# Performance work log

Hardware: AMD Instinct MI355X
Metric: run time of the kernel (lower is better)

The kernel has to match this reference:

```python
import jax, jax.numpy as jnp
import numpy as np
from jax import lax

B, S, T = 64, 64, 32
VE = VD = 32000
E = H = 256
L = 2


def _cell(x, h, c, Wih, Whh, b):
    # PyTorch LSTM gate order: i, f, g, o
    g = x @ Wih.T + h @ Whh.T + b  # [B, 4H]
    i, f, gg, o = jnp.split(g, 4, axis=-1)
    c2 = jax.nn.sigmoid(f) * c + jax.nn.sigmoid(i) * jnp.tanh(gg)
    h2 = jax.nn.sigmoid(o) * jnp.tanh(c2)
    return h2, c2


def _stack_step(x, h, c, Wih, Whh, b):
    # x: [B, E]; h, c: [L, B, H]. Stacked LSTM, dropout is identity at inference.
    hs, cs = [], []
    inp = x
    for l in range(h.shape[0]):
        h2, c2 = _cell(inp, h[l], c[l], Wih[l], Whh[l], b[l])
        hs.append(h2); cs.append(c2)
        inp = h2
    return jnp.stack(hs), jnp.stack(cs), inp


def _encode(tokens, emb, Wih, Whh, b):
    x = emb[tokens]  # [B, S, E]
    bsz = tokens.shape[0]
    h0 = jnp.zeros((L, bsz, H), x.dtype)
    c0 = jnp.zeros((L, bsz, H), x.dtype)

    def step(carry, xt):
        h, c = carry
        h, c, _ = _stack_step(xt, h, c, Wih, Whh, b)
        return (h, c), None

    (h, c), _ = lax.scan(step, (h0, c0), x.transpose(1, 0, 2))
    return h, c


def setup_inputs():
    key = jax.random.key(0)
    ks = jax.random.split(key, 12)
    sd = lambda k, shape: (jax.random.normal(k, shape, dtype=jnp.float32) * 0.05)
    return {
        "input_seq": jax.random.randint(ks[0], (B, S), 0, VE),
        "target_seq": jax.random.randint(ks[1], (B, T), 0, VD),
        "enc_emb": sd(ks[2], (VE, E)),
        "dec_emb": sd(ks[3], (VD, E)),
        "enc_Wih": sd(ks[4], (L, 4 * H, E)),
        "enc_Whh": sd(ks[5], (L, 4 * H, H)),
        "enc_b": sd(ks[6], (L, 4 * H)),
        "dec_Wih": sd(ks[7], (L, 4 * H, E)),
        "dec_Whh": sd(ks[8], (L, 4 * H, H)),
        "dec_b": sd(ks[9], (L, 4 * H)),
        "W_out": sd(ks[10], (VD, H)),
        "b_out": sd(ks[11], (VD,)),
    }


def reference(input_seq, target_seq, enc_emb, dec_emb, enc_Wih, enc_Whh, enc_b,
              dec_Wih, dec_Whh, dec_b, W_out, b_out):
    h, c = _encode(input_seq, enc_emb, enc_Wih, enc_Whh, enc_b)
    bsz, tlen = target_seq.shape
    # dec_in buffer; position 0 is BOS token target_seq[:, 0]; rest filled greedily
    buf0 = jnp.zeros((bsz, tlen), dtype=target_seq.dtype).at[:, 0].set(target_seq[:, 0])
    pos = jnp.arange(tlen)

    def outer(carry, t):
        h, c, buf = carry
        x = dec_emb[buf]  # [B, T, E] -- whole growing prefix re-fed, as in source

        def inner(carry, inp):
            hh, cc = carry
            xt, p = inp
            h2, c2, _ = _stack_step(xt, hh, cc, dec_Wih, dec_Whh, dec_b)
            m = p <= t  # only positions up to current prefix length update state
            hh = jnp.where(m, h2, hh)
            cc = jnp.where(m, c2, cc)
            return (hh, cc), None

        (h, c), _ = lax.scan(inner, (h, c), (x.transpose(1, 0, 2), pos))
        out_top = h[-1]  # LSTM output at last real position t
        pred = out_top @ W_out.T + b_out  # [B, V]
        nxt = jnp.argmax(pred, axis=-1).astype(buf.dtype)
        buf = buf.at[:, t + 1].set(nxt)
        return (h, c, buf), pred

    (_, _, _), preds = lax.scan(outer, (h, c, buf0), jnp.arange(tlen - 1))
    return preds.transpose(1, 0, 2)  # [B, T-1, V]
```

## Files before the change

### kernel.cpp

```cpp
#include <hip/hip_runtime.h>
#include <math.h>


#define B     64
#define SLEN  64
#define TLEN  32
#define HID   256
#define EMBD  256
#define G4    1024
#define VOC   32000
#define NPRED 31
#define FBASE 64
#define FS    16

typedef unsigned long long u64;

__device__ __forceinline__ float sigf(float x){ return 1.0f/(1.0f+__expf(-x)); }

__device__ __forceinline__ void gstoref(float* p, float v){
  __hip_atomic_store(p, v, __ATOMIC_RELAXED, __HIP_MEMORY_SCOPE_AGENT);
}
__device__ __forceinline__ void gstorei(int* p, int v){
  __hip_atomic_store(p, v, __ATOMIC_RELAXED, __HIP_MEMORY_SCOPE_AGENT);
}
__device__ __forceinline__ float gloadf(const float* p){
  return __hip_atomic_load(p, __ATOMIC_RELAXED, __HIP_MEMORY_SCOPE_AGENT);
}
__device__ __forceinline__ int gload32(const int* p){
  return __hip_atomic_load(p, __ATOMIC_RELAXED, __HIP_MEMORY_SCOPE_AGENT);
}

__global__ void k_zero(int* __restrict__ p){
  p[blockIdx.x*1024 + threadIdx.x] = 0;
}

__global__ __launch_bounds__(256) void k_tr(const float* __restrict__ src,
                                            float* __restrict__ dst){
  __shared__ float t[64][65];
  const int r0 = blockIdx.x*64, c0 = blockIdx.y*64;
  const int lr = threadIdx.x>>6, lc = threadIdx.x&63;
  #pragma unroll
  for (int i=0;i<16;i++){
    int r = lr + i*4;
    t[r][lc] = src[(size_t)(r0+r)*256 + c0+lc];
  }
  __syncthreads();
  #pragma unroll
  for (int i=0;i<16;i++){
    int c = lr + i*4;
    dst[(size_t)(c0+c)*1024 + r0+lc] = t[lc][c];
  }
}

__global__ __launch_bounds__(256) void k_xproj(
    const int* __restrict__ tok, int tok_stride, int pos0,
    const float* __restrict__ emb, const float* __restrict__ W,
    const float* __restrict__ b0, float* __restrict__ out)
{
  __shared__ float xT[128][64];
  const int tid  = threadIdx.x;
  const int lane = tid & 63;
  const int wv   = __builtin_amdgcn_readfirstlane(tid >> 6);
  const int pos  = pos0 + blockIdx.y;
  const int jbase= blockIdx.x*32 + wv*8;

  const int rS = tid >> 2, klane = tid & 3;
  const int tokrow = tok[rS*tok_stride + pos];
  const float* xsrc = emb + (size_t)tokrow*EMBD;

  float acc[8];
  #pragma unroll
  for (int jj=0;jj<8;jj++) acc[jj]=0.f;

  for (int c=0;c<2;c++){
    __syncthreads();
    #pragma unroll
    for (int i=0;i<32;i++){
      int k = klane + 4*i;
      xT[k][rS] = xsrc[c*128 + k];
    }
    __syncthreads();
    for (int kc=0;kc<8;kc++){
      float x[16];
      #pragma unroll
      for (int i=0;i<16;i++) x[i] = xT[kc*16+i][lane];
      #pragma unroll
      for (int jj=0;jj<8;jj++){
        const float* Wp = W + (size_t)(jbase+jj)*EMBD + c*128 + kc*16;
        float s = 0.f;
        #pragma unroll
        for (int i=0;i<16;i++) s += Wp[i]*x[i];
        acc[jj] += s;
      }
    }
  }
  #pragma unroll
  for (int jj=0;jj<8;jj++){
    int j = jbase+jj;
    out[((size_t)pos*64 + lane)*G4 + j] = acc[jj] + b0[j];
  }
}

__device__ __forceinline__ float4 dotpart(const float4* __restrict__ Wq,
                                          const float* __restrict__ hs,
                                          int kq, int jg){
  float ax=0.f, ay=0.f, az=0.f, aw=0.f;
  const float4* __restrict__ hq = (const float4*)(hs + (kq<<6));
  const float4* __restrict__ w  = Wq + (size_t)(kq<<6)*256 + jg;
  #pragma unroll 4
  for (int kk=0; kk<16; ++kk){
    float4 h4 = hq[kk];
    float4 w0 = w[0];
    float4 w1 = w[256];
    float4 w2 = w[512];
    float4 w3 = w[768];
    ax += w0.x*h4.x; ay += w0.y*h4.x; az += w0.z*h4.x; aw += w0.w*h4.x;
    ax += w1.x*h4.y; ay += w1.y*h4.y; az += w1.z*h4.y; aw += w1.w*h4.y;
    ax += w2.x*h4.z; ay += w2.y*h4.z; az += w2.z*h4.z; aw += w2.w*h4.z;
    ax += w3.x*h4.w; ay += w3.y*h4.w; az += w3.z*h4.w; aw += w3.w*h4.w;
    w += 1024;
  }
  return make_float4(ax,ay,az,aw);
}

__global__ __launch_bounds__(1024) void k_pipe(
    const float* __restrict__ xp, int nsteps,
    const float* __restrict__ WT0, const float* __restrict__ WT1i,
    const float* __restrict__ WT1h, const float* __restrict__ b1,
    float* __restrict__ h0P, float* __restrict__ h1P,
    float* __restrict__ c0P, float* __restrict__ c1P,
    float* __restrict__ h0R, float* __restrict__ p1R,
    int* __restrict__ fA, int* __restrict__ fB1, int* __restrict__ fB2,
    int fbase, int initzero)
{
  __shared__ __align__(16) float part[4][4096];
  __shared__ float xps[1024];
  __shared__ __align__(16) float hloc[256];
  __shared__ float padL[4096];
  const int tid  = threadIdx.x;
  const int kq   = tid >> 8, jg = tid & 255;
  const int role = blockIdx.x >> 6;
  const int r    = blockIdx.x & 63;
  if (nsteps < 0){ padL[tid] = xp[tid]; h0R[tid] = padL[tid ^ 1]; }

  if (role == 0){
    float c0 = 0.f;
    if (tid < HID){
      if (initzero){ c0 = 0.f; hloc[tid] = 0.f; }
      else { c0 = c0P[tid*64 + r]; hloc[tid] = h0P[tid*64 + r]; }
    }
    __syncthreads();
    const float4* W4 = (const float4*)WT0;
    for (int q = 0; q < nsteps; ++q){
      float xv = xp[((size_t)q*64 + r)*G4 + tid];
      if (tid == 0 && q >= 4){
        int tgt = fbase + q - 3, g = 0;
        while (gload32(fB1 + r*FS) < tgt && ++g < (1<<24)) {}
      }
      float4 a = dotpart(W4, hloc, kq, jg);
      xps[tid] = xv;
      *(float4*)&part[kq][jg<<2] = a;
      __syncthreads();
      if (tid < HID){
        float g0 = part[0][tid]+part[1][tid]+part[2][tid]+part[3][tid] + xps[tid];
        float g1 = part[0][HID+tid]+part[1][HID+tid]+part[2][HID+tid]+part[3][HID+tid] + xps[HID+tid];
        float g2 = part[0][2*HID+tid]+part[1][2*HID+tid]+part[2][2*HID+tid]+part[3][2*HID+tid] + xps[2*HID+tid];
        float g3 = part[0][3*HID+tid]+part[1][3*HID+tid]+part[2][3*HID+tid]+part[3][3*HID+tid] + xps[3*HID+tid];
        c0 = sigf(g1)*c0 + sigf(g0)*tanhf(g2);
        float h = sigf(g3)*tanhf(c0);
        hloc[tid] = h;
        gstoref(h0R + (q&3)*16384 + r*256 + tid, h);
        asm volatile("s_waitcnt vmcnt(0)" ::: "memory");
      }
      __syncthreads();
      if (tid == 0) gstorei(fA + r*FS, fbase + q + 1);
    }
    if (tid < HID){ c0P[tid*64 + r] = c0; h0P[tid*64 + r] = hloc[tid]; }
  }
  else if (role == 1){
    const float4* W4 = (const float4*)WT1i;
    for (int q = 0; q < nsteps; ++q){
      if (tid == 0){
        int tgt = fbase + q + 1, g = 0;
        while (gload32(fA + r*FS) < tgt && ++g < (1<<24)) {}
        if (q >= 4){
          int t2 = fbase + q - 3; g = 0;
          while (gload32(fB2 + r*FS) < t2 && ++g < (1<<24)) {}
        }
      }
      __syncthreads();
      if (tid < HID) hloc[tid] = gloadf(h0R + (q&3)*16384 + r*256 + tid);
      __syncthreads();
      float4 a = dotpart(W4, hloc, kq, jg);
      *(float4*)&part[kq][jg<<2] = a;
      __syncthreads();
      float p = part[0][tid]+part[1][tid]+part[2][tid]+part[3][tid];
      gstoref(p1R + (q&3)*65536 + r*1024 + tid, p);
      asm volatile("s_waitcnt vmcnt(0)" ::: "memory");
      __syncthreads();
      if (tid == 0) gstorei(fB1 + r*FS, fbase + q + 1);
    }
  }
  else {
    float c1 = 0.f, bb0=0.f, bb1=0.f, bb2=0.f, bb3=0.f;
    if (tid < HID){
      bb0 = b1[tid]; bb1 = b1[HID+tid]; bb2 = b1[2*HID+tid]; bb3 = b1[3*HID+tid];
      if (initzero){ c1 = 0.f; hloc[tid] = 0.f; }
      else { c1 = c1P[tid*64 + r]; hloc[tid] = h1P[tid*64 + r]; }
    }
    __syncthreads();
    const float4* W4 = (const float4*)WT1h;
    for (int q = 0; q < nsteps; ++q){
      if (tid == 0){
        int tgt = fbase + q + 1, g = 0;
        while (gload32(fB1 + r*FS) < tgt && ++g < (1<<24)) {}
      }
      __syncthreads();
      xps[tid] = gloadf(p1R + (q&3)*65536 + r*1024 + tid);
      asm volatile("s_waitcnt vmcnt(0)" ::: "memory");
      __syncthreads();
      if (tid == 0) gstorei(fB2 + r*FS, fbase + q + 1);
      float4 a = dotpart(W4, hloc, kq, jg);
      *(float4*)&part[kq][jg<<2] = a;
      __syncthreads();
      if (tid < HID){
        float g0 = part[0][tid]+part[1][tid]+part[2][tid]+part[3][tid] + xps[tid] + bb0;
        float g1 = part[0][HID+tid]+part[1][HID+tid]+part[2][HID+tid]+part[3][HID+tid] + xps[HID+tid] + bb1;
        float g2 = part[0][2*HID+tid]+part[1][2*HID+tid]+part[2][2*HID+tid]+part[3][2*HID+tid] + xps[2*HID+tid] + bb2;
        float g3 = part[0][3*HID+tid]+part[1][3*HID+tid]+part[2][3*HID+tid]+part[3][3*HID+tid] + xps[3*HID+tid] + bb3;
        c1 = sigf(g1)*c1 + sigf(g0)*tanhf(g2);
        float h = sigf(g3)*tanhf(c1);
        hloc[tid] = h;
        if (q == nsteps-1) h1P[tid*64 + r] = h;
      }
      __syncthreads();
    }
    if (tid < HID) c1P[tid*64 + r] = c1;
  }
}

__global__ __launch_bounds__(1024) void k_megadec(
    float* xp,
    const float* __restrict__ WT0, const float* __restrict__ WT1i,
    const float* __restrict__ WT1h, const float* __restrict__ b1,
    const float* __restrict__ Wih0, const float* __restrict__ b0,
    const float* __restrict__ emb,
    const float* __restrict__ Wout, const float* __restrict__ bout,
    float* __restrict__ dout,
    const float* __restrict__ h0P, const float* __restrict__ h1P,
    const float* __restrict__ c0P, const float* __restrict__ c1P,
    float* __restrict__ h0R, float* __restrict__ p1R, float* __restrict__ h1R,
    float* __restrict__ pPv, int* __restrict__ pPi,
    int* __restrict__ flags)
{
  __shared__ __align__(16) float part[4][4096];
  __shared__ float xps[1024];
  __shared__ __align__(16) float hloc[256];
  __shared__ int   iscr[1024];
  __shared__ float htp[256*65];

  int* fA = flags;          int* fB1 = flags + 1024;  int* fB2 = flags + 2048;
  int* fH = flags + 3072;   int* fP  = flags + 4096;  int* fX  = flags + 5120;

  const int tid  = threadIdx.x;
  const int lane = tid & 63;
  const int wv   = __builtin_amdgcn_readfirstlane(tid >> 6);
  const int kq   = tid >> 8, jg = tid & 255;
  const int xcd  = blockIdx.x & 7;
  const int role = xcd >> 1;
  const int r    = ((xcd & 1) << 5) | (blockIdx.x >> 3);

  if (role == 0){
    float c0 = 0.f;
    if (tid < HID){ c0 = c0P[tid*64 + r]; hloc[tid] = h0P[tid*64 + r]; }
    __syncthreads();
    const float4* W4 = (const float4*)WT0;
    int cum = 0;
    for (int t = 0; t < NPRED; ++t)
    for (int p = 0; p <= t; ++p, ++cum){
      if (wv == 0){
        if (lane == 0 && cum >= 4){
          int tgt = FBASE + cum - 3, g = 0;
          while (gload32(fB1 + r*FS) < tgt && ++g < (1<<24)) {}
        }
        if (p == t && t >= 1){
          int g = 0;
          while (!__all(gload32(fX + lane*FS) >= t) && ++g < (1<<24)) {}
        }
      }
      __syncthreads();
      const float* xa = xp + ((size_t)p*64 + r)*G4 + tid;
      float xv = (p == t) ? gloadf(xa) : *xa;
      float4 a = dotpart(W4, hloc, kq, jg);
      xps[tid] = xv;
      *(float4*)&part[kq][jg<<2] = a;
      __syncthreads();
      if (tid < HID){
        float g0 = part[0][tid]+part[1][tid]+part[2][tid]+part[3][tid] + xps[tid];
        float g1 = part[0][HID+tid]+part[1][HID+tid]+part[2][HID+tid]+part[3][HID+tid] + xps[HID+tid];
        float g2 = part[0][2*HID+tid]+part[1][2*HID+tid]+part[2][2*HID+tid]+part[3][2*HID+tid] + xps[2*HID+tid];
        float g3 = part[0][3*HID+tid]+part[1][3*HID+tid]+part[2][3*HID+tid]+part[3][3*HID+tid] + xps[3*HID+tid];
        c0 = sigf(g1)*c0 + sigf(g0)*tanhf(g2);
        float h = sigf(g3)*tanhf(c0);
        hloc[tid] = h;
        gstoref(h0R + (cum&3)*16384 + r*256 + tid, h);
        asm volatile("s_waitcnt vmcnt(0)" ::: "memory");
      }
      __syncthreads();
      if (tid == 0) gstorei(fA + r*FS, FBASE + cum + 1);
    }
  }
  else if (role == 1){
    const float4* W4 = (const float4*)WT1i;
    int cum = 0;
    for (int t = 0; t < NPRED; ++t)
    for (int p = 0; p <= t; ++p, ++cum){
      if (tid == 0){
        int tgt = FBASE + cum + 1, g = 0;
        while (gload32(fA + r*FS) < tgt && ++g < (1<<24)) {}
        if (cum >= 4){
          int t2 = FBASE + cum - 3; g = 0;
          while (gload32(fB2 + r*FS) < t2 && ++g < (1<<24)) {}
        }
      }
      __syncthreads();
      if (tid < HID) hloc[tid] = gloadf(h0R + (cum&3)*16384 + r*256 + tid);
      __syncthreads();
      float4 a = dotpart(W4, hloc, kq, jg);
      *(float4*)&part[kq][jg<<2] = a;
      __syncthreads();
      float pp = part[0][tid]+part[1][tid]+part[2][tid]+part[3][tid];
      gstoref(p1R + (cum&3)*65536 + r*1024 + tid, pp);
      asm volatile("s_waitcnt vmcnt(0)" ::: "memory");
      __syncthreads();
      if (tid == 0) gstorei(fB1 + r*FS, FBASE + cum + 1);
    }
  }
  else if (role == 2){
    float c1 = 0.f, bb0=0.f, bb1=0.f, bb2=0.f, bb3=0.f;
    if (tid < HID){
      bb0 = b1[tid]; bb1 = b1[HID+tid]; bb2 = b1[2*HID+tid]; bb3 = b1[3*HID+tid];
      c1 = c1P[tid*64 + r]; hloc[tid] = h1P[tid*64 + r];
    }
    __syncthreads();
    const float4* W4 = (const float4*)WT1h;
    int cum = 0;
    for (int t = 0; t < NPRED; ++t)
    for (int p = 0; p <= t; ++p, ++cum){
      if (tid == 0){
        int tgt = FBASE + cum + 1, g = 0;
        while (gload32(fB1 + r*FS) < tgt && ++g < (1<<24)) {}
      }
      __syncthreads();
      xps[tid] = gloadf(p1R + (cum&3)*65536 + r*1024 + tid);
      asm volatile("s_waitcnt vmcnt(0)" ::: "memory");
      __syncthreads();
      if (tid == 0) gstorei(fB2 + r*FS, FBASE + cum + 1);
      float4 a = dotpart(W4, hloc, kq, jg);
      *(float4*)&part[kq][jg<<2] = a;
      __syncthreads();
      if (tid < HID){
        float g0 = part[0][tid]+part[1][tid]+part[2][tid]+part[3][tid] + xps[tid] + bb0;
        float g1 = part[0][HID+tid]+part[1][HID+tid]+part[2][HID+tid]+part[3][HID+tid] + xps[HID+tid] + bb1;
        float g2 = part[0][2*HID+tid]+part[1][2*HID+tid]+part[2][2*HID+tid]+part[3][2*HID+tid] + xps[2*HID+tid] + bb2;
        float g3 = part[0][3*HID+tid]+part[1][3*HID+tid]+part[2][3*HID+tid]+part[3][3*HID+tid] + xps[3*HID+tid] + bb3;
        c1 = sigf(g1)*c1 + sigf(g0)*tanhf(g2);
        float h = sigf(g3)*tanhf(c1);
        hloc[tid] = h;
      }
      __syncthreads();
      if (p == t){
        if (tid == 0 && t >= 2){
          int g = 0;
          while (gload32(fP) < t - 1 && ++g < (1<<24)) {}
        }
        if (wv == 1 && t >= 2){
          int g = 0;
          while (!__all(gload32(fP + lane*FS) >= t-1) && ++g < (1<<24)) {}
        }
        __syncthreads();
        if (tid < HID){
          gstoref(h1R + (t&1)*16384 + r*256 + tid, hloc[tid]);
          asm volatile("s_waitcnt vmcnt(0)" ::: "memory");
        }
        __syncthreads();
        if (tid == 0) gstorei(fH + r*FS, t + 1);
      }
    }
  }
  else {
    const int v  = r;
    const int v0 = v * 500;
    const int rr = tid >> 4;
    const int jl = tid & 15;
    const float b0v = b0[v*16 + jl];

    for (int t = 0; t < NPRED; ++t){
      if (wv == 0){
        int g = 0;
        while (!__all(gload32(fH + lane*FS) >= t+1) && ++g < (1<<24))
          __builtin_amdgcn_s_sleep(8);
      }
      __syncthreads();
      {
        const float* src = h1R + (size_t)(t&1)*16384;
        #pragma unroll
        for (int i=0;i<16;i++){
          int idx = tid + i*1024;
          float vl = gloadf(src + idx);
          htp[(idx & 255)*65 + (idx >> 8)] = vl;
        }
      }
      __syncthreads();
      float best = -INFINITY; int bi = 0x7fffffff;
      for (int ib = 0; ib < 4; ++ib){
        float acc[8];
        #pragma unroll
        for (int jj=0;jj<8;jj++){
          int i = ib*8+jj;
          acc[jj] = (wv + 16*i < 500) ? bout[v0 + wv + 16*i] : 0.f;
        }
        for (int kc = 0; kc < 16; ++kc){
          float x[16];
          #pragma unroll
          for (int u=0;u<16;u++) x[u] = htp[(kc*16+u)*65 + lane];
          #pragma unroll
          for (int jj=0;jj<8;jj++){
            int i = ib*8+jj;
            if (wv + 16*i < 500){
              const float* Wp = Wout + (size_t)(v0 + wv + 16*i)*HID + kc*16;
              #pragma unroll
              for (int u=0;u<16;u++) acc[jj] += Wp[u]*x[u];
            }
          }
        }
        #pragma unroll
        for (int jj=0;jj<8;jj++){
          int i = ib*8+jj;
          if (wv + 16*i < 500){
            int vv = v0 + wv + 16*i;
            dout[((size_t)lane*NPRED + t)*VOC + vv] = acc[jj];
            if (acc[jj] > best){ best = acc[jj]; bi = vv; }
          }
        }
      }
      xps[wv*64 + lane] = best; iscr[wv*64 + lane] = bi;
      __syncthreads();
      if (wv == 0){
        float bb = xps[lane]; int bbi = iscr[lane];
        #pragma unroll
        for (int w=1; w<16; w++){
          float vl = xps[w*64+lane]; int ii = iscr[w*64+lane];
          if (vl > bb || (vl == bb && ii < bbi)){ bb = vl; bbi = ii; }
        }
        gstoref(pPv + (t&1)*4096 + v*64 + lane, bb);
        gstorei(pPi + (t&1)*4096 + v*64 + lane, bbi);
        asm volatile("s_waitcnt vmcnt(0)" ::: "memory");
      }
      __syncthreads();
      if (tid == 0) gstorei(fP + v*FS, t + 1);
      if (t == NPRED-1) continue;

      if (wv == 0){
        int g = 0;
        while (!__all(gload32(fP + lane*FS) >= t+1) && ++g < (1<<24)) {}
        float bb = -INFINITY; int bbi = 0x7fffffff;
        for (int vs = 0; vs < 64; ++vs){
          float vl = gloadf(pPv + (t&1)*4096 + vs*64 + lane);
          int  ii  = gload32(pPi + (t&1)*4096 + vs*64 + lane);
          if (vl > bb || (vl == bb && ii < bbi)){ bb = vl; bbi = ii; }
        }
        iscr[lane] = bbi;
      }
      __syncthreads();
      {
        #pragma unroll
        for (int i=0;i<16;i++){
          int idx = tid + i*1024;
          int k2 = idx >> 6, r2 = idx & 63;
          int tk = iscr[r2];
          htp[k2*65 + r2] = emb[(size_t)tk*EMBD + k2];
        }
      }
      __syncthreads();
      {
        int j = v*16 + jl;
        const float* Wj = Wih0 + (size_t)j*EMBD;
        float acc = b0v;
        #pragma unroll 16
        for (int k2=0;k2<256;k2++) acc += Wj[k2]*htp[k2*65 + rr];
        gstoref(xp + ((size_t)(t+1)*64 + rr)*G4 + v*16 + jl, acc);
        asm volatile("s_waitcnt vmcnt(0)" ::: "memory");
      }
      __syncthreads();
      if (tid == 0) gstorei(fX + v*FS, t + 1);
    }
  }
}

extern "C" void kernel_launch(void* const* d_in, const int* in_sizes, int n_in,
                              void* d_out, int out_size, void* d_ws, size_t ws_size,
                              hipStream_t stream)
{
  const int*   input_seq  = (const int*)d_in[0];
  const int*   target_seq = (const int*)d_in[1];
  const float* enc_emb = (const float*)d_in[2];
  const float* dec_emb = (const float*)d_in[3];
  const float* enc_Wih = (const float*)d_in[4];
  const float* enc_Whh = (const float*)d_in[5];
  const float* enc_b   = (const float*)d_in[6];
  const float* dec_Wih = (const float*)d_in[7];
  const float* dec_Whh = (const float*)d_in[8];
  const float* dec_b   = (const float*)d_in[9];
  const float* W_out   = (const float*)d_in[10];
  const float* b_out   = (const float*)d_in[11];
  float* out = (float*)d_out;

  float* ws   = (float*)d_ws;
  float* xp_e = ws;
  float* xp_d = xp_e + (size_t)SLEN*64*G4;
  float* h0P  = xp_d + (size_t)TLEN*64*G4;
  float* h1P  = h0P + HID*64;
  float* c0P  = h1P + HID*64;
  float* c1P  = c0P + HID*64;
  float* h0R  = c1P + HID*64;
  float* p1R  = h0R + 4*16384;
  float* h1R  = p1R + 4*65536;
  float* pPv  = h1R + 2*16384;
  int*   pPi  = (int*)(pPv + 2*4096);
  int*   flags= (int*)(pPi + 2*4096);
  float* WT0  = (float*)(flags + 6144);
  float* WT1i = WT0  + HID*G4;
  float* WT1h = WT1i + HID*G4;

  k_zero<<<6, 1024, 0, stream>>>(flags);

  dim3 trg(16, 4);
  k_tr<<<trg, 256, 0, stream>>>(enc_Whh,                   WT0);
  k_tr<<<trg, 256, 0, stream>>>(enc_Wih + (size_t)G4*EMBD, WT1i);
  k_tr<<<trg, 256, 0, stream>>>(enc_Whh + (size_t)G4*HID,  WT1h);
  k_xproj<<<dim3(32, SLEN), 256, 0, stream>>>(input_seq, SLEN, 0, enc_emb,
        enc_Wih, enc_b, xp_e);
  k_pipe<<<192, 1024, 0, stream>>>(xp_e, SLEN,
        WT0, WT1i, WT1h, enc_b + G4,
        h0P, h1P, c0P, c1P, h0R, p1R,
        flags, flags + 1024, flags + 2048, 0, 1);

  k_tr<<<trg, 256, 0, stream>>>(dec_Whh,                   WT0);
  k_tr<<<trg, 256, 0, stream>>>(dec_Wih + (size_t)G4*EMBD, WT1i);
  k_tr<<<trg, 256, 0, stream>>>(dec_Whh + (size_t)G4*HID,  WT1h);
  k_xproj<<<dim3(32, 1), 256, 0, stream>>>(target_seq, TLEN, 0, dec_emb,
        dec_Wih, dec_b, xp_d);

  k_megadec<<<256, 1024, 0, stream>>>(xp_d,
        WT0, WT1i, WT1h, dec_b + G4,
        dec_Wih, dec_b, dec_emb, W_out, b_out, out,
        h0P, h1P, c0P, c1P,
        h0R, p1R, h1R, pPv, pPi, flags);
}
```

Measured before the change: 9.060 ms.

## Funnel cross-block flag polling through a single aggregator block

Many-to-many flag polling between the recurrence blocks and the 64 vocabulary/projection blocks is replaced by aggregation in block v==0. That block alone polls all fH, fP and fX flags, then publishes single go flags (fGo, fTok, fXGo) plus the argmax token vector. The other blocks spin on one word instead of 64 strided flags, cutting global polling traffic and contention. The cost is an extra serial hop through block 0 on each handoff, which adds latency on the critical path.

Result: slower. 9.494 ms (+4.8%).

```diff
diff --git a/kernel.cpp b/kernel.cpp
--- a/kernel.cpp
+++ b/kernel.cpp
@@ -259,8 +259,10 @@
   __shared__ int   iscr[1024];
   __shared__ float htp[256*65];
 
-  int* fA = flags;          int* fB1 = flags + 1024;  int* fB2 = flags + 2048;
-  int* fH = flags + 3072;   int* fP  = flags + 4096;  int* fX  = flags + 5120;
+  int* fA  = flags;          int* fB1 = flags + 1024;  int* fB2 = flags + 2048;
+  int* fH  = flags + 3072;   int* fP  = flags + 4096;  int* fX  = flags + 5120;
+  int* fGo = flags + 6144;   int* fTok= flags + 6160;  int* fXGo= flags + 6176;
+  int* tokG= flags + 6656;
 
   const int tid  = threadIdx.x;
   const int lane = tid & 63;
@@ -278,17 +280,18 @@
     int cum = 0;
     for (int t = 0; t < NPRED; ++t)
     for (int p = 0; p <= t; ++p, ++cum){
-      if (wv == 0){
-        if (lane == 0 && cum >= 4){
+      if (tid == 0){
+        if (cum >= 4){
           int tgt = FBASE + cum - 3, g = 0;
           while (gload32(fB1 + r*FS) < tgt && ++g < (1<<24)) {}
         }
         if (p == t && t >= 1){
           int g = 0;
-          while (!__all(gload32(fX + lane*FS) >= t) && ++g < (1<<24)) {}
-        }
-      }
-      __syncthreads();
+          while (gload32(fXGo) < t && ++g < (1<<24)) {}
+        }
+      }
+      __syncthreads();
+      asm volatile("" ::: "memory");
       const float* xa = xp + ((size_t)p*64 + r)*G4 + tid;
       float xv = (p == t) ? gloadf(xa) : *xa;
       float4 a = dotpart(W4, hloc, kq, jg);
@@ -372,13 +375,10 @@
       if (p == t){
         if (tid == 0 && t >= 2){
           int g = 0;
-          while (gload32(fP) < t - 1 && ++g < (1<<24)) {}
-        }
-        if (wv == 1 && t >= 2){
-          int g = 0;
-          while (!__all(gload32(fP + lane*FS) >= t-1) && ++g < (1<<24)) {}
-        }
-        __syncthreads();
+          while (gload32(fTok) < t - 1 && ++g < (1<<24)) {}
+        }
+        __syncthreads();
+        asm volatile("" ::: "memory");
         if (tid < HID){
           gstoref(h1R + (t&1)*16384 + r*256 + tid, hloc[tid]);
           asm volatile("s_waitcnt vmcnt(0)" ::: "memory");
@@ -396,12 +396,23 @@
     const float b0v = b0[v*16 + jl];
 
     for (int t = 0; t < NPRED; ++t){
-      if (wv == 0){
-        int g = 0;
-        while (!__all(gload32(fH + lane*FS) >= t+1) && ++g < (1<<24))
-          __builtin_amdgcn_s_sleep(8);
-      }
-      __syncthreads();
+      if (v == 0){
+        if (wv == 0){
+          int g = 0;
+          while (!__all(gload32(fH + lane*FS) >= t+1) && ++g < (1<<24))
+            __builtin_amdgcn_s_sleep(4);
+        }
+        __syncthreads();
+        if (tid == 0) gstorei(fGo, t + 1);
+      } else {
+        if (tid == 0){
+          int g = 0;
+          while (gload32(fGo) < t + 1 && ++g < (1<<24))
+            __builtin_amdgcn_s_sleep(8);
+        }
+        __syncthreads();
+      }
+      asm volatile("" ::: "memory");
       {
         const float* src = h1R + (size_t)(t&1)*16384;
         #pragma unroll
@@ -461,18 +472,33 @@
       if (tid == 0) gstorei(fP + v*FS, t + 1);
       if (t == NPRED-1) continue;
 
-      if (wv == 0){
-        int g = 0;
-        while (!__all(gload32(fP + lane*FS) >= t+1) && ++g < (1<<24)) {}
-        float bb = -INFINITY; int bbi = 0x7fffffff;
-        for (int vs = 0; vs < 64; ++vs){
-          float vl = gloadf(pPv + (t&1)*4096 + vs*64 + lane);
-          int  ii  = gload32(pPi + (t&1)*4096 + vs*64 + lane);
-          if (vl > bb || (vl == bb && ii < bbi)){ bb = vl; bbi = ii; }
-        }
-        iscr[lane] = bbi;
-      }
-      __syncthreads();
+      if (v == 0){
+        if (wv == 0){
+          int g = 0;
+          while (!__all(gload32(fP + lane*FS) >= t+1) && ++g < (1<<24)) {}
+          float bb = -INFINITY; int bbi = 0x7fffffff;
+          for (int vs = 0; vs < 64; ++vs){
+            float vl = gloadf(pPv + (t&1)*4096 + vs*64 + lane);
+            int  ii  = gload32(pPi + (t&1)*4096 + vs*64 + lane);
+            if (vl > bb || (vl == bb && ii < bbi)){ bb = vl; bbi = ii; }
+          }
+          iscr[lane] = bbi;
+          gstorei(tokG + lane, bbi);
+          asm volatile("s_waitcnt vmcnt(0)" ::: "memory");
+        }
+        __syncthreads();
+        if (tid == 0) gstorei(fTok, t + 1);
+      } else {
+        if (tid == 0){
+          int g = 0;
+          while (gload32(fTok) < t + 1 && ++g < (1<<24))
+            __builtin_amdgcn_s_sleep(2);
+        }
+        __syncthreads();
+        asm volatile("" ::: "memory");
+        if (tid < 64) iscr[tid] = gload32(tokG + tid);
+        __syncthreads();
+      }
       {
         #pragma unroll
         for (int i=0;i<16;i++){
@@ -494,6 +520,14 @@
       }
       __syncthreads();
       if (tid == 0) gstorei(fX + v*FS, t + 1);
+      if (v == 0){
+        if (wv == 0){
+          int g = 0;
+          while (!__all(gload32(fX + lane*FS) >= t+1) && ++g < (1<<24)) {}
+        }
+        __syncthreads();
+        if (tid == 0) gstorei(fXGo, t + 1);
+      }
     }
   }
 }
@@ -529,11 +563,11 @@
   float* pPv  = h1R + 2*16384;
   int*   pPi  = (int*)(pPv + 2*4096);
   int*   flags= (int*)(pPi + 2*4096);
-  float* WT0  = (float*)(flags + 6144);
+  float* WT0  = (float*)(flags + 7168);
   float* WT1i = WT0  + HID*G4;
   float* WT1h = WT1i + HID*G4;
 
-  k_zero<<<6, 1024, 0, stream>>>(flags);
+  k_zero<<<7, 1024, 0, stream>>>(flags);
 
   dim3 trg(16, 4);
   k_tr<<<trg, 256, 0, stream>>>(enc_Whh,                   WT0);
```
